# Kernel tuning notes

Hardware: AMD Instinct MI355X
Metric: run time of the kernel (lower is better)

## Reference

```python
import jax, jax.numpy as jnp
import numpy as np

B, S, R, E, H = 2, 2048, 128, 2048, 16
D = E // H  # head_dim = 128


def _ste(x, q):
    # straight-through estimator: forward=q, backward=identity
    return x + jax.lax.stop_gradient(q - x)


def quant_weight(w):
    # BitNet b1.58-style ternary weight quantization with mean-abs scale
    scale = jnp.clip(jnp.mean(jnp.abs(w)), 1e-5, None)
    q = jnp.clip(jnp.round(w / scale), -1.0, 1.0) * scale
    return _ste(w, q)


def quant_act(x):
    # per-token 8-bit absmax activation quantization
    s = 127.0 / jnp.clip(jnp.max(jnp.abs(x), axis=-1, keepdims=True), 1e-5, None)
    q = jnp.clip(jnp.round(x * s), -128.0, 127.0) / s
    return _ste(x, q)


def quantized_linear(x, w):
    # dequantized low-bit matmul: Xq @ Wq^T
    return quant_act(x) @ quant_weight(w).T


def setup_inputs() -> dict:
    key = jax.random.key(0)
    ks = jax.random.split(key, 8)
    sc = 1.0 / np.sqrt(E)
    return {
        "x": jax.random.normal(ks[0], (B, S, E), dtype=jnp.float32),
        "reasoning_tokens": jax.random.normal(ks[1], (B, R, E), dtype=jnp.float32),
        "q_w": jax.random.normal(ks[2], (E, E), dtype=jnp.float32) * sc,
        "k_w": jax.random.normal(ks[3], (E, E), dtype=jnp.float32) * sc,
        "v_w": jax.random.normal(ks[4], (E, E), dtype=jnp.float32) * sc,
        "out_w": jax.random.normal(ks[5], (E, E), dtype=jnp.float32) * sc,
        "out_b": jnp.zeros((E,), dtype=jnp.float32),
    }


def _heads(t):
    b, s, _ = t.shape
    return t.reshape(b, s, H, D).transpose(0, 2, 1, 3)  # [B,H,S,D]


def reference(x, reasoning_tokens, q_w, k_w, v_w, out_w, out_b):
    b, s, e = x.shape
    # quantized QKV projections (dequant + matmul)
    q = _heads(quantized_linear(x, q_w))
    k = _heads(quantized_linear(x, k_w))
    v = _heads(quantized_linear(x, v_w))
    # reasoning tokens go through the UNquantized projections (per source)
    rk = _heads(reasoning_tokens @ k_w.T)
    rv = _heads(reasoning_tokens @ v_w.T)
    k = jnp.concatenate([k, rk], axis=2)  # [B,H,S+R,D]
    v = jnp.concatenate([v, rv], axis=2)
    scores = jnp.einsum('bhqd,bhkd->bhqk', q, k) / np.sqrt(D).astype(np.float32)
    attn = jax.nn.softmax(scores, axis=-1)
    o = jnp.einsum('bhqk,bhkd->bhqd', attn, v)
    o = o.transpose(0, 2, 1, 3).reshape(b, s, e)
    return o @ out_w.T + out_b
```

## Files before the change

### kernel.cpp

```cpp
#include <hip/hip_runtime.h>


typedef __bf16 bf16;
typedef __bf16 bf16x8 __attribute__((ext_vector_type(8)));
typedef float  f32x4  __attribute__((ext_vector_type(4)));
typedef int    i32x4  __attribute__((ext_vector_type(4)));
typedef char   char8  __attribute__((ext_vector_type(8)));

#define B_   2
#define S_   2048
#define R_   128
#define E_   2048
#define H_   16
#define D_   128
#define NKV  2176
#define HKV  1088
#define NTOK 4096
#define KDIM 2048

typedef const __attribute__((address_space(1))) void* gas_ptr;
typedef __attribute__((address_space(3))) void*       las_ptr;

__device__ __forceinline__ void load_lds16(const void* g, void* l) {
  __builtin_amdgcn_global_load_lds((gas_ptr)g, (las_ptr)l, 16, 0, 0);
}

__global__ __launch_bounds__(256) void abs_sum_k(
    const float* __restrict__ w0, const float* __restrict__ w1,
    const float* __restrict__ w2, double* wsD) {
  int z = blockIdx.y;
  const float* w = z == 0 ? w0 : (z == 1 ? w1 : w2);
  int tid = threadIdx.x;
  size_t base = ((size_t)blockIdx.x * 256 + tid) * 8;
  f32x4 a = *(const f32x4*)(w + base);
  f32x4 b = *(const f32x4*)(w + base + 4);
  float s = 0.f;
#pragma unroll
  for (int j = 0; j < 4; j++) s += fabsf(a[j]) + fabsf(b[j]);
  double d = (double)s;
#pragma unroll
  for (int m = 1; m < 64; m <<= 1) d += __shfl_xor(d, m);
  __shared__ double red[4];
  if ((tid & 63) == 0) red[tid >> 6] = d;
  __syncthreads();
  if (tid == 0) atomicAdd(&wsD[z], red[0] + red[1] + red[2] + red[3]);
}

__global__ __launch_bounds__(256) void prep_k(
    const float* __restrict__ qw, const float* __restrict__ kw,
    const float* __restrict__ vw, const float* __restrict__ ow,
    const float* __restrict__ rt, const double* __restrict__ wsD, float* wsF,
    char* __restrict__ TQ8, char* __restrict__ TK8, char* __restrict__ TV8,
    bf16* __restrict__ KWb, bf16* __restrict__ VWb, bf16* __restrict__ OWb,
    bf16* __restrict__ RTb) {
  int y = blockIdx.y;
  if (y < 3) {
    const float* w = y == 0 ? qw : (y == 1 ? kw : vw);
    char* t        = y == 0 ? TQ8 : (y == 1 ? TK8 : TV8);
    float scale = (float)fmax(wsD[y] * (1.0 / 4194304.0), 1e-5);
    if (blockIdx.x == 0 && threadIdx.x == 0) wsF[y] = scale;
    size_t base = ((size_t)blockIdx.x * 256 + threadIdx.x) * 8;
    f32x4 a = *(const f32x4*)(w + base);
    f32x4 b = *(const f32x4*)(w + base + 4);
    float rs = 1.0f / scale;
    char8 o;
#pragma unroll
    for (int j = 0; j < 8; j++) {
      float v = j < 4 ? a[j] : b[j - 4];
      float q = rintf(v * rs);
      q = fminf(fmaxf(q, -1.f), 1.f);
      o[j] = (char)(int)q;
    }
    *(char8*)(t + base) = o;
  } else {
    if (y == 6 && blockIdx.x >= 256) return;
    const float* src = y == 3 ? kw : (y == 4 ? vw : (y == 5 ? ow : rt));
    bf16* dst        = y == 3 ? KWb : (y == 4 ? VWb : (y == 5 ? OWb : RTb));
    size_t i = ((size_t)blockIdx.x * 256 + threadIdx.x) * 8;
    f32x4 a = *(const f32x4*)(src + i);
    f32x4 b = *(const f32x4*)(src + i + 4);
    bf16x8 o;
#pragma unroll
    for (int j = 0; j < 4; j++) { o[j] = (bf16)a[j]; o[j + 4] = (bf16)b[j]; }
    *(bf16x8*)(dst + i) = o;
  }
}

__global__ __launch_bounds__(256) void actq_k(
    const float* __restrict__ x, char* __restrict__ xq,
    float* __restrict__ aScale) {
  int row = blockIdx.x, tid = threadIdx.x;
  const float* xr = x + (size_t)row * E_;
  f32x4 a = *(const f32x4*)(xr + tid * 8);
  f32x4 b = *(const f32x4*)(xr + tid * 8 + 4);
  float am = 0.f;
#pragma unroll
  for (int j = 0; j < 4; j++) am = fmaxf(am, fmaxf(fabsf(a[j]), fabsf(b[j])));
#pragma unroll
  for (int m = 1; m < 64; m <<= 1) am = fmaxf(am, __shfl_xor(am, m));
  __shared__ float red[4];
  if ((tid & 63) == 0) red[tid >> 6] = am;
  __syncthreads();
  float mx = fmaxf(fmaxf(red[0], red[1]), fmaxf(red[2], red[3]));
  float maxC = fmaxf(mx, 1e-5f);
  float s = 127.0f / maxC;
  char8 o;
#pragma unroll
  for (int j = 0; j < 8; j++) {
    float v = j < 4 ? a[j] : b[j - 4];
    float q = rintf(v * s);
    q = fminf(fmaxf(q, -128.f), 127.f);
    o[j] = (char)(int)q;
  }
  *(char8*)(xq + (size_t)row * E_ + tid * 8) = o;
  if (tid == 0) aScale[row] = maxC / 127.0f;
}

__device__ __forceinline__ void gemm_core(const bf16* Arow, const bf16* Brow,
                                          bf16* As, bf16* Bs, int tid,
                                          f32x4 acc[4][4]) {
  int wave = tid >> 6, lane = tid & 63, quad = lane >> 4, l16 = lane & 15;
  int wm = wave >> 1, wn = wave & 1;
  const char* aT = (const char*)Arow;
  const char* bT = (const char*)Brow;
  int c1 = tid + 256;
  size_t aO0 = (size_t)(tid >> 2) * (KDIM * 2) + (size_t)(tid & 3) * 16;
  size_t aO1 = (size_t)(c1 >> 2) * (KDIM * 2) + (size_t)(c1 & 3) * 16;
  char* AsB = (char*)As;
  char* BsB = (char*)Bs;
  int wofs = wave * 1024;
  for (int k0 = 0; k0 < KDIM; k0 += 32) {
    __syncthreads();
    load_lds16(aT + aO0, AsB + wofs);
    load_lds16(aT + aO1, AsB + 4096 + wofs);
    load_lds16(bT + aO0, BsB + wofs);
    load_lds16(bT + aO1, BsB + 4096 + wofs);
    aT += 64;
    bT += 64;
    __syncthreads();
    bf16x8 af[4], bfr[4];
#pragma unroll
    for (int mt = 0; mt < 4; mt++)
      af[mt] = *(const bf16x8*)(As + (wm * 64 + mt * 16 + l16) * 32 + quad * 8);
#pragma unroll
    for (int nt = 0; nt < 4; nt++)
      bfr[nt] = *(const bf16x8*)(Bs + (wn * 64 + nt * 16 + l16) * 32 + quad * 8);
#pragma unroll
    for (int mt = 0; mt < 4; mt++)
#pragma unroll
      for (int nt = 0; nt < 4; nt++)
        acc[mt][nt] = __builtin_amdgcn_mfma_f32_16x16x32_bf16(
            af[mt], bfr[nt], acc[mt][nt], 0, 0, 0);
  }
}

__device__ __forceinline__ void gemm_core_i8(const char* Arow, const char* Brow,
                                             char* As, char* Bs, int tid,
                                             i32x4 acc[4][4]) {
  int wave = tid >> 6, lane = tid & 63, quad = lane >> 4, l16 = lane & 15;
  int wm = wave >> 1, wn = wave & 1;
  int s0 = tid, s1 = tid + 256;
  int r0 = s0 >> 2, r1 = s1 >> 2;
  size_t aO0 = (size_t)r0 * KDIM + (size_t)((s0 & 3) ^ (r0 & 3)) * 16;
  size_t aO1 = (size_t)r1 * KDIM + (size_t)((s1 & 3) ^ (r1 & 3)) * 16;
  const char* aT = Arow;
  const char* bT = Brow;
  int wofs = wave * 1024;
  int cs = (quad ^ (l16 & 3)) * 16;
  for (int k0 = 0; k0 < KDIM; k0 += 64) {
    __syncthreads();
    load_lds16(aT + aO0, As + wofs);
    load_lds16(aT + aO1, As + 4096 + wofs);
    load_lds16(bT + aO0, Bs + wofs);
    load_lds16(bT + aO1, Bs + 4096 + wofs);
    aT += 64;
    bT += 64;
    __syncthreads();
    i32x4 af[4], bfr[4];
#pragma unroll
    for (int mt = 0; mt < 4; mt++)
      af[mt] = *(const i32x4*)(As + (wm * 64 + mt * 16 + l16) * 64 + cs);
#pragma unroll
    for (int nt = 0; nt < 4; nt++)
      bfr[nt] = *(const i32x4*)(Bs + (wn * 64 + nt * 16 + l16) * 64 + cs);
#pragma unroll
    for (int mt = 0; mt < 4; mt++)
#pragma unroll
      for (int nt = 0; nt < 4; nt++)
        acc[mt][nt] = __builtin_amdgcn_mfma_i32_16x16x64_i8(
            af[mt], bfr[nt], acc[mt][nt], 0, 0, 0);
  }
}

__global__ __launch_bounds__(256) void gemm_proj(
    const char* __restrict__ XQ8, const char* __restrict__ TQ8,
    const char* __restrict__ TK8, const char* __restrict__ TV8,
    const bf16* __restrict__ RTb, const bf16* __restrict__ KWb,
    const bf16* __restrict__ VWb, const float* __restrict__ asc,
    const float* __restrict__ wsF, bf16* __restrict__ QB,
    bf16* __restrict__ KB, bf16* __restrict__ VT) {
  __shared__ char As[8192];
  __shared__ char Bs[8192];
  int tid = threadIdx.x;
  int lane = tid & 63, quad = lane >> 4, l16 = lane & 15;
  int wm = (tid >> 6) >> 1, wn = (tid >> 6) & 1;

  if (blockIdx.y < 32) {
    int m0 = blockIdx.x * 128, n0 = blockIdx.y * 128;
    bool isQ = n0 < 2048;
    bool isRsn = m0 >= NTOK;
    if (isQ && isRsn) return;
    if (!isRsn) {
      const char* Bm = isQ ? (TQ8 + (size_t)n0 * KDIM)
                           : (TK8 + (size_t)(n0 - 2048) * KDIM);
      float sW = isQ ? wsF[0] : wsF[1];
      i32x4 acc[4][4];
      const i32x4 iz = {0, 0, 0, 0};
#pragma unroll
      for (int i = 0; i < 4; i++)
#pragma unroll
        for (int j = 0; j < 4; j++) acc[i][j] = iz;
      gemm_core_i8(XQ8 + (size_t)m0 * KDIM, Bm, As, Bs, tid, acc);
#pragma unroll
      for (int mt = 0; mt < 4; mt++) {
        int mB = m0 + wm * 64 + mt * 16 + quad * 4;
#pragma unroll
        for (int nt = 0; nt < 4; nt++) {
          int n = n0 + wn * 64 + nt * 16 + l16;
          int nn = n & 2047, h = nn >> 7, d = nn & 127;
#pragma unroll
          for (int r = 0; r < 4; r++) {
            int m = mB + r;
            float v = (float)acc[mt][nt][r] * asc[m] * sW;
            int tb = m >> 11, ts = m & 2047;
            if (isQ)
              QB[((size_t)((tb * 16 + h) * S_ + ts)) * 128 + d] = (bf16)v;
            else
              KB[((size_t)((tb * 16 + h) * NKV + ts)) * 128 + d] = (bf16)v;
          }
        }
      }
    } else {
      f32x4 acc[4][4];
      const f32x4 fz = {0.f, 0.f, 0.f, 0.f};
#pragma unroll
      for (int i = 0; i < 4; i++)
#pragma unroll
        for (int j = 0; j < 4; j++) acc[i][j] = fz;
      gemm_core(RTb + (size_t)(m0 - NTOK) * KDIM,
                KWb + (size_t)(n0 - 2048) * KDIM, (bf16*)As, (bf16*)Bs, tid,
                acc);
#pragma unroll
      for (int mt = 0; mt < 4; mt++) {
        int mB = m0 + wm * 64 + mt * 16 + quad * 4;
#pragma unroll
        for (int nt = 0; nt < 4; nt++) {
          int n = n0 + wn * 64 + nt * 16 + l16;
          int nn = n & 2047, h = nn >> 7, d = nn & 127;
#pragma unroll
          for (int r = 0; r < 4; r++) {
            int j = mB + r - NTOK;
            int tb = j >> 7, ts = 2048 + (j & 127);
            KB[((size_t)((tb * 16 + h) * NKV + ts)) * 128 + d] =
                (bf16)acc[mt][nt][r];
          }
        }
      }
    }
  } else {
    int m0 = (blockIdx.y - 32) * 128, n0 = blockIdx.x * 128;
    bool isRsn = n0 >= NTOK;
    if (!isRsn) {
      i32x4 acc[4][4];
      const i32x4 iz = {0, 0, 0, 0};
#pragma unroll
      for (int i = 0; i < 4; i++)
#pragma unroll
        for (int j = 0; j < 4; j++) acc[i][j] = iz;
      gemm_core_i8(TV8 + (size_t)m0 * KDIM, XQ8 + (size_t)n0 * KDIM, As, Bs,
                   tid, acc);
#pragma unroll
      for (int mt = 0; mt < 4; mt++) {
        int mB = m0 + wm * 64 + mt * 16 + quad * 4;
#pragma unroll
        for (int nt = 0; nt < 4; nt++) {
          int n = n0 + wn * 64 + nt * 16 + l16;
          float sb = asc[n] * wsF[2];
          int tb = n >> 11, ts = n & 2047;
#pragma unroll
          for (int r = 0; r < 4; r++) {
            int m = mB + r, h = m >> 7, d = m & 127;
            VT[((size_t)((tb * 16 + h) * 128 + d)) * NKV + ts] =
                (bf16)((float)acc[mt][nt][r] * sb);
          }
        }
      }
    } else {
      f32x4 acc[4][4];
      const f32x4 fz = {0.f, 0.f, 0.f, 0.f};
#pragma unroll
      for (int i = 0; i < 4; i++)
#pragma unroll
        for (int j = 0; j < 4; j++) acc[i][j] = fz;
      gemm_core(VWb + (size_t)m0 * KDIM, RTb + (size_t)(n0 - NTOK) * KDIM,
                (bf16*)As, (bf16*)Bs, tid, acc);
#pragma unroll
      for (int mt = 0; mt < 4; mt++) {
        int mB = m0 + wm * 64 + mt * 16 + quad * 4;
#pragma unroll
        for (int nt = 0; nt < 4; nt++) {
          int n = n0 + wn * 64 + nt * 16 + l16;
          int j = n - NTOK, tb = j >> 7, ts = 2048 + (j & 127);
#pragma unroll
          for (int r = 0; r < 4; r++) {
            int m = mB + r, h = m >> 7, d = m & 127;
            VT[((size_t)((tb * 16 + h) * 128 + d)) * NKV + ts] =
                (bf16)acc[mt][nt][r];
          }
        }
      }
    }
  }
}

__global__ __launch_bounds__(256) void gemm_out(
    const bf16* __restrict__ A, const bf16* __restrict__ Bm,
    const float* __restrict__ bias, float* __restrict__ out) {
  __shared__ bf16 As[128 * 32];
  __shared__ bf16 Bs[128 * 32];
  int m0 = blockIdx.x * 128, n0 = blockIdx.y * 128;
  int tid = threadIdx.x;
  int lane = tid & 63, quad = lane >> 4, l16 = lane & 15;
  int wm = (tid >> 6) >> 1, wn = (tid >> 6) & 1;

  f32x4 acc[4][4];
  const f32x4 fz = {0.f, 0.f, 0.f, 0.f};
#pragma unroll
  for (int i = 0; i < 4; i++)
#pragma unroll
    for (int j = 0; j < 4; j++) acc[i][j] = fz;
  gemm_core(A + (size_t)m0 * KDIM, Bm + (size_t)n0 * KDIM, As, Bs, tid, acc);

#pragma unroll
  for (int mt = 0; mt < 4; mt++) {
    int mB = m0 + wm * 64 + mt * 16 + quad * 4;
#pragma unroll
    for (int nt = 0; nt < 4; nt++) {
      int n = n0 + wn * 64 + nt * 16 + l16;
      float bv = bias[n];
#pragma unroll
      for (int r = 0; r < 4; r++)
        out[(size_t)(mB + r) * E_ + n] = acc[mt][nt][r] + bv;
    }
  }
}

__global__ __launch_bounds__(256) void attn_k(
    const bf16* __restrict__ q, const bf16* __restrict__ k,
    const bf16* __restrict__ vt, bf16* __restrict__ Op,
    float* __restrict__ lp) {
  __shared__ bf16 Ks[64 * 128];
  __shared__ bf16 Vs[128 * 64];
  __shared__ bf16 Ps[128 * 64];
  const float SC = 0.08838834764831845f;
  const float SHIFT = 12.0f;
  int tid = threadIdx.x;
  int wave = tid >> 6, lane = tid & 63, quad = lane >> 4, l16 = lane & 15;
  int bh = blockIdx.y, q0 = blockIdx.x * 128;
  int kv0 = blockIdx.z * HKV;

  const bf16* qb = q + ((size_t)bh * S_ + q0) * D_;
  const char* kb = (const char*)(k + (size_t)bh * NKV * D_);
  const char* vb = (const char*)(vt + (size_t)bh * D_ * NKV);

  bf16x8 qf[2][4];
#pragma unroll
  for (int qt = 0; qt < 2; qt++)
#pragma unroll
    for (int ds = 0; ds < 4; ds++)
      qf[qt][ds] = *(const bf16x8*)(qb +
                   (size_t)(wave * 32 + qt * 16 + l16) * D_ + ds * 32 + quad * 8);

  const f32x4 fz = {0.f, 0.f, 0.f, 0.f};
  f32x4 oa[2][8];
#pragma unroll
  for (int i = 0; i < 2; i++)
#pragma unroll
    for (int j = 0; j < 8; j++) oa[i][j] = fz;
  float lsum[2][4];
#pragma unroll
  for (int i = 0; i < 2; i++)
#pragma unroll
    for (int r = 0; r < 4; r++) lsum[i][r] = 0.f;

  char* KsB = (char*)Ks;
  char* VsB = (char*)Vs;
  char* PsB = (char*)Ps;

  int kRow[4], kC[4], vRow[4], vC[4];
#pragma unroll
  for (int i = 0; i < 4; i++) {
    int slot = i * 256 + tid;
    kRow[i] = slot >> 4;
    kC[i] = (slot & 15) ^ (kRow[i] & 15);
    vRow[i] = slot >> 3;
    vC[i] = (slot & 7) ^ (vRow[i] & 7);
  }
  int wofs = wave * 1024;

  for (int kv = kv0; kv < kv0 + HKV; kv += 64) {
    __syncthreads();
#pragma unroll
    for (int i = 0; i < 4; i++)
      load_lds16(kb + (size_t)(kv + kRow[i]) * 256 + kC[i] * 16,
                 KsB + i * 4096 + wofs);
#pragma unroll
    for (int i = 0; i < 4; i++)
      load_lds16(vb + (size_t)vRow[i] * (NKV * 2) + (size_t)kv * 2 + vC[i] * 16,
                 VsB + i * 4096 + wofs);
    __syncthreads();

    f32x4 s[2][4];
#pragma unroll
    for (int i = 0; i < 2; i++)
#pragma unroll
      for (int j = 0; j < 4; j++) s[i][j] = fz;
#pragma unroll
    for (int ds = 0; ds < 4; ds++) {
      bf16x8 kf[4];
#pragma unroll
      for (int kt = 0; kt < 4; kt++) {
        int row = kt * 16 + l16;
        int c = (ds * 4 + quad) ^ (row & 15);
        kf[kt] = *(const bf16x8*)(KsB + row * 256 + c * 16);
      }
#pragma unroll
      for (int qt = 0; qt < 2; qt++)
#pragma unroll
        for (int kt = 0; kt < 4; kt++)
          s[qt][kt] = __builtin_amdgcn_mfma_f32_16x16x32_bf16(
              qf[qt][ds], kf[kt], s[qt][kt], 0, 0, 0);
    }

#pragma unroll
    for (int qt = 0; qt < 2; qt++)
#pragma unroll
      for (int kt = 0; kt < 4; kt++)
#pragma unroll
        for (int r = 0; r < 4; r++)
          s[qt][kt][r] = __expf(s[qt][kt][r] * SC - SHIFT);
#pragma unroll
    for (int qt = 0; qt < 2; qt++)
#pragma unroll
      for (int r = 0; r < 4; r++)
        lsum[qt][r] += (s[qt][0][r] + s[qt][1][r]) + (s[qt][2][r] + s[qt][3][r]);

#pragma unroll
    for (int qt = 0; qt < 2; qt++)
#pragma unroll
      for (int kt = 0; kt < 4; kt++)
#pragma unroll
        for (int r = 0; r < 4; r++) {
          int row = wave * 32 + qt * 16 + quad * 4 + r;
          int col = kt * 16 + l16;
          int c = (col >> 3) ^ (row & 7);
          *(bf16*)(PsB + row * 128 + c * 16 + (col & 7) * 2) =
              (bf16)s[qt][kt][r];
        }
    __syncthreads();

#pragma unroll
    for (int ks = 0; ks < 2; ks++) {
      bf16x8 pf[2], vf[8];
#pragma unroll
      for (int qt = 0; qt < 2; qt++) {
        int row = wave * 32 + qt * 16 + l16;
        int c = (ks * 4 + quad) ^ (row & 7);
        pf[qt] = *(const bf16x8*)(PsB + row * 128 + c * 16);
      }
#pragma unroll
      for (int dt = 0; dt < 8; dt++) {
        int row = dt * 16 + l16;
        int c = (ks * 4 + quad) ^ (row & 7);
        vf[dt] = *(const bf16x8*)(VsB + row * 128 + c * 16);
      }
#pragma unroll
      for (int qt = 0; qt < 2; qt++)
#pragma unroll
        for (int dt = 0; dt < 8; dt++)
          oa[qt][dt] = __builtin_amdgcn_mfma_f32_16x16x32_bf16(
              pf[qt], vf[dt], oa[qt][dt], 0, 0, 0);
    }
  }

  size_t zofs = (size_t)blockIdx.z * ((size_t)B_ * H_ * S_);
#pragma unroll
  for (int qt = 0; qt < 2; qt++) {
#pragma unroll
    for (int r = 0; r < 4; r++) {
      float l = lsum[qt][r];
#pragma unroll
      for (int msk = 1; msk < 16; msk <<= 1) l += __shfl_xor(l, msk);
      if (l16 == 0) {
        int srow = q0 + wave * 32 + qt * 16 + quad * 4 + r;
        lp[zofs + (size_t)bh * S_ + srow] = l;
      }
    }
#pragma unroll
    for (int dt = 0; dt < 8; dt++)
#pragma unroll
      for (int r = 0; r < 4; r++) {
        int srow = q0 + wave * 32 + qt * 16 + quad * 4 + r;
        int col = dt * 16 + l16;
        Op[(zofs + (size_t)bh * S_ + srow) * 128 + col] = (bf16)oa[qt][dt][r];
      }
  }
}

__global__ __launch_bounds__(256) void combine_k(
    const bf16* __restrict__ Op, const float* __restrict__ lp,
    bf16* __restrict__ OB) {
  int m = blockIdx.x, t = threadIdx.x;
  int b = m >> 11, s = m & 2047;
  int idx = t * 8, h = idx >> 7, d = idx & 127;
  size_t rofs = ((size_t)(b * 16 + h) * S_ + s);
  const size_t Z = (size_t)B_ * H_ * S_;
  float rl = 1.0f / (lp[rofs] + lp[Z + rofs]);
  bf16x8 o0 = *(const bf16x8*)(Op + rofs * 128 + d);
  bf16x8 o1 = *(const bf16x8*)(Op + (Z + rofs) * 128 + d);
  bf16x8 o;
#pragma unroll
  for (int j = 0; j < 8; j++) o[j] = (bf16)(((float)o0[j] + (float)o1[j]) * rl);
  *(bf16x8*)(OB + (size_t)m * E_ + idx) = o;
}

static constexpr size_t O_ASC = 256;
static constexpr size_t O_XQ8 = 32768;
static constexpr size_t O_RTB = O_XQ8 + 8388608;
static constexpr size_t O_TQ8 = O_RTB + 1048576;
static constexpr size_t O_TK8 = O_TQ8 + 4194304;
static constexpr size_t O_TV8 = O_TK8 + 4194304;
static constexpr size_t O_KWB = O_TV8 + 4194304;
static constexpr size_t O_VWB = O_KWB + 8388608;
static constexpr size_t O_OWB = O_VWB + 8388608;
static constexpr size_t O_QB  = O_OWB + 8388608;
static constexpr size_t O_KB  = O_QB + 16777216;
static constexpr size_t O_VT  = O_KB + 17825792;
static constexpr size_t WS_NEED = O_VT + 17825792;
static constexpr size_t O_OP = O_XQ8;
static constexpr size_t O_LP = O_XQ8 + 33554432;
static constexpr size_t O_OB = O_QB;

extern "C" void kernel_launch(void* const* d_in, const int* in_sizes, int n_in,
                              void* d_out, int out_size, void* d_ws,
                              size_t ws_size, hipStream_t stream) {
  const float* x  = (const float*)d_in[0];
  const float* rt = (const float*)d_in[1];
  const float* qw = (const float*)d_in[2];
  const float* kw = (const float*)d_in[3];
  const float* vw = (const float*)d_in[4];
  const float* ow = (const float*)d_in[5];
  const float* ob = (const float*)d_in[6];
  char* ws = (char*)d_ws;
  if (ws_size < WS_NEED) return;

  double* wsD = (double*)ws;
  float* wsF  = (float*)(ws + 64);
  float* asc  = (float*)(ws + O_ASC);
  char* XQ8 = ws + O_XQ8;
  bf16* RTb = (bf16*)(ws + O_RTB);
  char* TQ8 = ws + O_TQ8;
  char* TK8 = ws + O_TK8;
  char* TV8 = ws + O_TV8;
  bf16* KWb = (bf16*)(ws + O_KWB);
  bf16* VWb = (bf16*)(ws + O_VWB);
  bf16* OWb = (bf16*)(ws + O_OWB);
  bf16* QB  = (bf16*)(ws + O_QB);
  bf16* KB  = (bf16*)(ws + O_KB);
  bf16* VT  = (bf16*)(ws + O_VT);
  bf16* Op  = (bf16*)(ws + O_OP);
  float* lp = (float*)(ws + O_LP);
  bf16* OB  = (bf16*)(ws + O_OB);
  float* out = (float*)d_out;

  hipMemsetAsync(ws, 0, 64, stream);
  abs_sum_k<<<dim3(2048, 3), 256, 0, stream>>>(qw, kw, vw, wsD);
  prep_k<<<dim3(2048, 7), 256, 0, stream>>>(qw, kw, vw, ow, rt, wsD, wsF,
                                            TQ8, TK8, TV8, KWb, VWb, OWb, RTb);
  actq_k<<<4096, 256, 0, stream>>>(x, XQ8, asc);

  gemm_proj<<<dim3(34, 48), 256, 0, stream>>>(XQ8, TQ8, TK8, TV8, RTb, KWb,
                                              VWb, asc, wsF, QB, KB, VT);

  attn_k<<<dim3(16, 32, 2), 256, 0, stream>>>(QB, KB, VT, Op, lp);
  combine_k<<<4096, 256, 0, stream>>>(Op, lp, OB);

  gemm_out<<<dim3(32, 16), 256, 0, stream>>>(OB, OWb, ob, out);
}
```

Measured before the change: 536.0 us.

## Compute transposed S=K·Q^T with 32x32 MFMA and keep P in registers

Rewrites the attention inner loop to use 32x32x16 MFMA. It computes the scores transposed, so each lane owns one query column and its softmax weights stay in registers. The P tile is rearranged across lane halves with shuffles and fed straight into the PV MFMA. This removes the LDS P buffer, its writes and reads, and one barrier per KV tile, and it simplifies the row-sum reduction. In exchange it adds cross-lane shuffles and more register pressure from the 16-wide accumulators.

```diff
diff --git a/kernel.cpp b/kernel.cpp
--- a/kernel.cpp
+++ b/kernel.cpp
@@ -2,8 +2,10 @@
 
 
 typedef __bf16 bf16;
+typedef __bf16 bf16x4 __attribute__((ext_vector_type(4)));
 typedef __bf16 bf16x8 __attribute__((ext_vector_type(8)));
 typedef float  f32x4  __attribute__((ext_vector_type(4)));
+typedef float  f32x16 __attribute__((ext_vector_type(16)));
 typedef int    i32x4  __attribute__((ext_vector_type(4)));
 typedef char   char8  __attribute__((ext_vector_type(8)));
 
@@ -361,41 +363,31 @@
     float* __restrict__ lp) {
   __shared__ bf16 Ks[64 * 128];
   __shared__ bf16 Vs[128 * 64];
-  __shared__ bf16 Ps[128 * 64];
   const float SC = 0.08838834764831845f;
   const float SHIFT = 12.0f;
   int tid = threadIdx.x;
-  int wave = tid >> 6, lane = tid & 63, quad = lane >> 4, l16 = lane & 15;
+  int wave = tid >> 6, lane = tid & 63, hh = lane >> 5, l31 = lane & 31;
   int bh = blockIdx.y, q0 = blockIdx.x * 128;
   int kv0 = blockIdx.z * HKV;
 
-  const bf16* qb = q + ((size_t)bh * S_ + q0) * D_;
+  const bf16* qb = q + ((size_t)bh * S_ + q0 + wave * 32 + l31) * D_;
   const char* kb = (const char*)(k + (size_t)bh * NKV * D_);
   const char* vb = (const char*)(vt + (size_t)bh * D_ * NKV);
 
-  bf16x8 qf[2][4];
-#pragma unroll
-  for (int qt = 0; qt < 2; qt++)
-#pragma unroll
-    for (int ds = 0; ds < 4; ds++)
-      qf[qt][ds] = *(const bf16x8*)(qb +
-                   (size_t)(wave * 32 + qt * 16 + l16) * D_ + ds * 32 + quad * 8);
-
-  const f32x4 fz = {0.f, 0.f, 0.f, 0.f};
-  f32x4 oa[2][8];
-#pragma unroll
-  for (int i = 0; i < 2; i++)
-#pragma unroll
-    for (int j = 0; j < 8; j++) oa[i][j] = fz;
-  float lsum[2][4];
-#pragma unroll
-  for (int i = 0; i < 2; i++)
-#pragma unroll
-    for (int r = 0; r < 4; r++) lsum[i][r] = 0.f;
+  bf16x8 qf[8];
+#pragma unroll
+  for (int ds = 0; ds < 8; ds++)
+    qf[ds] = *(const bf16x8*)(qb + ds * 16 + hh * 8);
+
+  f32x16 oa[4];
+#pragma unroll
+  for (int i = 0; i < 4; i++)
+#pragma unroll
+    for (int r = 0; r < 16; r++) oa[i][r] = 0.f;
+  float lsum = 0.f;
 
   char* KsB = (char*)Ks;
   char* VsB = (char*)Vs;
-  char* PsB = (char*)Ps;
 
   int kRow[4], kC[4], vRow[4], vC[4];
 #pragma unroll
@@ -420,101 +412,70 @@
                  VsB + i * 4096 + wofs);
     __syncthreads();
 
-    f32x4 s[2][4];
-#pragma unroll
-    for (int i = 0; i < 2; i++)
-#pragma unroll
-      for (int j = 0; j < 4; j++) s[i][j] = fz;
-#pragma unroll
-    for (int ds = 0; ds < 4; ds++) {
-      bf16x8 kf[4];
-#pragma unroll
-      for (int kt = 0; kt < 4; kt++) {
-        int row = kt * 16 + l16;
-        int c = (ds * 4 + quad) ^ (row & 15);
-        kf[kt] = *(const bf16x8*)(KsB + row * 256 + c * 16);
-      }
-#pragma unroll
-      for (int qt = 0; qt < 2; qt++)
-#pragma unroll
-        for (int kt = 0; kt < 4; kt++)
-          s[qt][kt] = __builtin_amdgcn_mfma_f32_16x16x32_bf16(
-              qf[qt][ds], kf[kt], s[qt][kt], 0, 0, 0);
+#pragma unroll
+    for (int kb2 = 0; kb2 < 2; kb2++) {
+      f32x16 st;
+#pragma unroll
+      for (int r = 0; r < 16; r++) st[r] = 0.f;
+      int krow = kb2 * 32 + l31;
+#pragma unroll
+      for (int ds = 0; ds < 8; ds++) {
+        int c0 = ds * 2 + hh;
+        bf16x8 kf = *(const bf16x8*)(KsB + krow * 256 +
+                                     ((c0 ^ (krow & 15)) * 16));
+        st = __builtin_amdgcn_mfma_f32_32x32x16_bf16(kf, qf[ds], st, 0, 0, 0);
+      }
+      union {
+        bf16 b[16];
+        int w[8];
+      } pu;
+#pragma unroll
+      for (int r = 0; r < 16; r++) {
+        float e = __expf(st[r] * SC - SHIFT);
+        lsum += e;
+        pu.b[r] = (bf16)e;
+      }
+#pragma unroll
+      for (int w16 = 0; w16 < 2; w16++) {
+        int w0 = pu.w[4 * w16 + 0], w1 = pu.w[4 * w16 + 1];
+        int w2 = pu.w[4 * w16 + 2], w3 = pu.w[4 * w16 + 3];
+        int s0 = __shfl_xor(w0, 32), s1 = __shfl_xor(w1, 32);
+        int s2 = __shfl_xor(w2, 32), s3 = __shfl_xor(w3, 32);
+        union {
+          int w[4];
+          bf16x8 v;
+        } fu;
+        fu.w[0] = hh ? s2 : w0;
+        fu.w[1] = hh ? s3 : w1;
+        fu.w[2] = hh ? w2 : s0;
+        fu.w[3] = hh ? w3 : s1;
+#pragma unroll
+        for (int db = 0; db < 4; db++) {
+          int vrow = db * 32 + l31;
+          int c0 = kb2 * 4 + w16 * 2 + hh;
+          bf16x8 vf = *(const bf16x8*)(VsB + vrow * 128 +
+                                       ((c0 ^ (vrow & 7)) * 16));
+          oa[db] = __builtin_amdgcn_mfma_f32_32x32x16_bf16(vf, fu.v, oa[db],
+                                                           0, 0, 0);
+        }
+      }
     }
-
-#pragma unroll
-    for (int qt = 0; qt < 2; qt++)
-#pragma unroll
-      for (int kt = 0; kt < 4; kt++)
-#pragma unroll
-        for (int r = 0; r < 4; r++)
-          s[qt][kt][r] = __expf(s[qt][kt][r] * SC - SHIFT);
-#pragma unroll
-    for (int qt = 0; qt < 2; qt++)
-#pragma unroll
-      for (int r = 0; r < 4; r++)
-        lsum[qt][r] += (s[qt][0][r] + s[qt][1][r]) + (s[qt][2][r] + s[qt][3][r]);
-
-#pragma unroll
-    for (int qt = 0; qt < 2; qt++)
-#pragma unroll
-      for (int kt = 0; kt < 4; kt++)
-#pragma unroll
-        for (int r = 0; r < 4; r++) {
-          int row = wave * 32 + qt * 16 + quad * 4 + r;
-          int col = kt * 16 + l16;
-          int c = (col >> 3) ^ (row & 7);
-          *(bf16*)(PsB + row * 128 + c * 16 + (col & 7) * 2) =
-              (bf16)s[qt][kt][r];
-        }
-    __syncthreads();
-
-#pragma unroll
-    for (int ks = 0; ks < 2; ks++) {
-      bf16x8 pf[2], vf[8];
-#pragma unroll
-      for (int qt = 0; qt < 2; qt++) {
-        int row = wave * 32 + qt * 16 + l16;
-        int c = (ks * 4 + quad) ^ (row & 7);
-        pf[qt] = *(const bf16x8*)(PsB + row * 128 + c * 16);
-      }
-#pragma unroll
-      for (int dt = 0; dt < 8; dt++) {
-        int row = dt * 16 + l16;
-        int c = (ks * 4 + quad) ^ (row & 7);
-        vf[dt] = *(const bf16x8*)(VsB + row * 128 + c * 16);
-      }
-#pragma unroll
-      for (int qt = 0; qt < 2; qt++)
-#pragma unroll
-        for (int dt = 0; dt < 8; dt++)
-          oa[qt][dt] = __builtin_amdgcn_mfma_f32_16x16x32_bf16(
-              pf[qt], vf[dt], oa[qt][dt], 0, 0, 0);
+  }
+
+  float lred = lsum + __shfl_xor(lsum, 32);
+  size_t zofs = (size_t)blockIdx.z * ((size_t)B_ * H_ * S_);
+  size_t rbase = zofs + (size_t)bh * S_ + q0 + wave * 32 + l31;
+  if (lane < 32) lp[rbase] = lred;
+#pragma unroll
+  for (int db = 0; db < 4; db++)
+#pragma unroll
+    for (int g = 0; g < 4; g++) {
+      int d = 8 * g + 4 * hh + 32 * db;
+      bf16x4 o4;
+#pragma unroll
+      for (int r = 0; r < 4; r++) o4[r] = (bf16)oa[db][4 * g + r];
+      *(bf16x4*)(Op + rbase * 128 + d) = o4;
     }
-  }
-
-  size_t zofs = (size_t)blockIdx.z * ((size_t)B_ * H_ * S_);
-#pragma unroll
-  for (int qt = 0; qt < 2; qt++) {
-#pragma unroll
-    for (int r = 0; r < 4; r++) {
-      float l = lsum[qt][r];
-#pragma unroll
-      for (int msk = 1; msk < 16; msk <<= 1) l += __shfl_xor(l, msk);
-      if (l16 == 0) {
-        int srow = q0 + wave * 32 + qt * 16 + quad * 4 + r;
-        lp[zofs + (size_t)bh * S_ + srow] = l;
-      }
-    }
-#pragma unroll
-    for (int dt = 0; dt < 8; dt++)
-#pragma unroll
-      for (int r = 0; r < 4; r++) {
-        int srow = q0 + wave * 32 + qt * 16 + quad * 4 + r;
-        int col = dt * 16 + l16;
-        Op[(zofs + (size_t)bh * S_ + srow) * 128 + col] = (bf16)oa[qt][dt][r];
-      }
-  }
 }
 
 __global__ __launch_bounds__(256) void combine_k(
```

New measurement: 523.8 us. 1.02x faster.
